# Kernel tuning notes

Hardware: AMD Instinct MI355X
Metric: run time of the kernel (lower is better)

## Reference

```python
import jax, jax.numpy as jnp
import numpy as np

B, N, F_IN, F_OUT = 8, 2048, 256, 256


def setup_inputs() -> dict:
    key = jax.random.key(0)
    k1, k2, k3, k4 = jax.random.split(key, 4)
    x = jax.random.normal(k1, (B, N, F_IN), dtype=jnp.float32)
    adj = jax.random.uniform(k2, (B, N, N), dtype=jnp.float32)
    W = jax.random.normal(k3, (F_IN, F_OUT), dtype=jnp.float32) * (1.0 / np.sqrt(F_IN))
    b = jax.random.normal(k4, (F_OUT,), dtype=jnp.float32)
    return {"x": x, "adj": adj, "W": W, "b": b}


def reference(x, adj, W, b):
    # GCN with dense adjacency: A_hat = A + I (fill_value=1.0, improved=False)
    n = adj.shape[-1]
    adj = adj + jnp.eye(n, dtype=adj.dtype)[None, :, :]
    deg = adj.sum(axis=-1)                       # [B, N]
    deg_inv_sqrt = deg ** -0.5
    deg_inv_sqrt = jnp.where(jnp.isinf(deg_inv_sqrt), 0.0, deg_inv_sqrt)
    # D^{-1/2} A D^{-1/2} via row/col broadcast (same math as diag bmm)
    adj_norm = deg_inv_sqrt[:, :, None] * adj * deg_inv_sqrt[:, None, :]
    h = jnp.einsum('bnf,fo->bno', x, W)          # linear, no bias
    out = jnp.einsum('bnm,bmo->bno', adj_norm, h)
    return out + b
```

## Files before the change

kernel.cpp:

```cpp
#include <hip/hip_runtime.h>
#include <hip/hip_bf16.h>

#define BB 8
#define NN 2048
#define FF 256
#define NT (NN / 64)

typedef __attribute__((ext_vector_type(8))) short short8;
typedef __attribute__((ext_vector_type(4))) short short4v;
typedef __attribute__((ext_vector_type(4))) float f32x4;
typedef __hip_bfloat16 bf16;

__device__ inline short f2bf(float x) {
  unsigned u = __builtin_bit_cast(unsigned, x);
  unsigned r = (u + 0x7fffu + ((u >> 16) & 1u)) >> 16;
  return (short)r;
}

__device__ inline void gl2lds16(const void* g, void* l) {
  __builtin_amdgcn_global_load_lds((const __attribute__((address_space(1))) void*)g,
                                   (__attribute__((address_space(3))) void*)l, 16, 0, 0);
}

__global__ __launch_bounds__(256)
void degconv_wt_kernel(const float* __restrict__ adj, const float* __restrict__ W,
                       float* __restrict__ dis, bf16* __restrict__ WT,
                       bf16* __restrict__ adjBF) {
  if (blockIdx.x >= BB * NN / 4) {
    int t2 = (blockIdx.x - BB * NN / 4) * 256 + threadIdx.x;
    int k = t2 >> 6, oc = (t2 & 63) * 4;
    float4 v = *reinterpret_cast<const float4*>(W + (size_t)k * FF + oc);
    *reinterpret_cast<short*>(WT + (size_t)(oc + 0) * FF + k) = f2bf(v.x);
    *reinterpret_cast<short*>(WT + (size_t)(oc + 1) * FF + k) = f2bf(v.y);
    *reinterpret_cast<short*>(WT + (size_t)(oc + 2) * FF + k) = f2bf(v.z);
    *reinterpret_cast<short*>(WT + (size_t)(oc + 3) * FF + k) = f2bf(v.w);
    return;
  }
  int wid = threadIdx.x >> 6, lane = threadIdx.x & 63;
  int row = blockIdx.x * 4 + wid;
  const float4* a4 = reinterpret_cast<const float4*>(adj + (size_t)row * NN);
  float4 v[8];
  float s = 0.f;
#pragma unroll
  for (int i = 0; i < 4; i++) {
    v[2 * i]     = a4[i * 128 + 2 * lane];
    v[2 * i + 1] = a4[i * 128 + 2 * lane + 1];
    s += v[2*i].x + v[2*i].y + v[2*i].z + v[2*i].w
       + v[2*i+1].x + v[2*i+1].y + v[2*i+1].z + v[2*i+1].w;
  }
#pragma unroll
  for (int off = 1; off < 64; off <<= 1) s += __shfl_xor(s, off, 64);
  float d = rsqrtf(s + 1.0f);
  if (lane == 0) dis[row] = d;
  int rb = row & (NN - 1);
#pragma unroll
  for (int i = 0; i < 8; i++) {
    int dd = rb - ((i >> 1) * 512 + 8 * lane + 4 * (i & 1));
    v[i].x += (dd == 0) ? 1.0f : 0.0f;
    v[i].y += (dd == 1) ? 1.0f : 0.0f;
    v[i].z += (dd == 2) ? 1.0f : 0.0f;
    v[i].w += (dd == 3) ? 1.0f : 0.0f;
  }
  bf16* orow = adjBF + (size_t)row * NN;
#pragma unroll
  for (int i = 0; i < 4; i++) {
    short8 w;
    w[0] = f2bf(v[2*i].x * d);   w[1] = f2bf(v[2*i].y * d);
    w[2] = f2bf(v[2*i].z * d);   w[3] = f2bf(v[2*i].w * d);
    w[4] = f2bf(v[2*i+1].x * d); w[5] = f2bf(v[2*i+1].y * d);
    w[6] = f2bf(v[2*i+1].z * d); w[7] = f2bf(v[2*i+1].w * d);
    *reinterpret_cast<short8*>(orow + i * 512 + 8 * lane) = w;
  }
}

__global__ __launch_bounds__(256)
void gemm1_kernel(const float* __restrict__ x, const bf16* __restrict__ WT,
                  const float* __restrict__ dis, bf16* __restrict__ gT) {
  __shared__ bf16 lA[128][40];
  __shared__ bf16 lB[128][40];
  int bid = blockIdx.x;
  int mtile = bid & 127, otile = bid >> 7;
  int m0 = mtile * 128, o0 = otile * 128;
  int t = threadIdx.x, wid = t >> 6, lane = t & 63;
  int wr = wid >> 1, wc = wid & 1;
  int srow = t >> 1, sseg = t & 1;
  const int r16 = lane & 15, kb = lane >> 4;

  f32x4 acc[4][4];
#pragma unroll
  for (int i = 0; i < 4; i++)
#pragma unroll
    for (int j = 0; j < 4; j++) acc[i][j] = (f32x4){0.f, 0.f, 0.f, 0.f};

  for (int k0 = 0; k0 < FF; k0 += 32) {
    {
      const float4* ap = reinterpret_cast<const float4*>(
          x + (size_t)(m0 + srow) * FF + k0 + sseg * 16);
      float arr[16];
      float4 v0 = ap[0], v1 = ap[1], v2 = ap[2], v3 = ap[3];
      arr[0]=v0.x; arr[1]=v0.y; arr[2]=v0.z; arr[3]=v0.w;
      arr[4]=v1.x; arr[5]=v1.y; arr[6]=v1.z; arr[7]=v1.w;
      arr[8]=v2.x; arr[9]=v2.y; arr[10]=v2.z; arr[11]=v2.w;
      arr[12]=v3.x; arr[13]=v3.y; arr[14]=v3.z; arr[15]=v3.w;
      short8 w0, w1;
#pragma unroll
      for (int e = 0; e < 8; e++) { w0[e] = f2bf(arr[e]); w1[e] = f2bf(arr[8 + e]); }
      *reinterpret_cast<short8*>(&lA[srow][sseg * 16]) = w0;
      *reinterpret_cast<short8*>(&lA[srow][sseg * 16 + 8]) = w1;
    }
    {
      const short8* bp = reinterpret_cast<const short8*>(
          WT + (size_t)(o0 + srow) * FF + k0 + sseg * 16);
      *reinterpret_cast<short8*>(&lB[srow][sseg * 16]) = bp[0];
      *reinterpret_cast<short8*>(&lB[srow][sseg * 16 + 8]) = bp[1];
    }
    __syncthreads();
    short8 af[4], bfr[4];
#pragma unroll
    for (int mf = 0; mf < 4; mf++)
      af[mf] = *reinterpret_cast<const short8*>(&lA[wr * 64 + mf * 16 + r16][kb * 8]);
#pragma unroll
    for (int nf = 0; nf < 4; nf++)
      bfr[nf] = *reinterpret_cast<const short8*>(&lB[wc * 64 + nf * 16 + r16][kb * 8]);
#pragma unroll
    for (int mf = 0; mf < 4; mf++)
#pragma unroll
      for (int nf = 0; nf < 4; nf++)
        acc[mf][nf] = __builtin_amdgcn_mfma_f32_16x16x32_bf16(af[mf], bfr[nf], acc[mf][nf], 0, 0, 0);
    __syncthreads();
  }

  int b = m0 >> 11;
#pragma unroll
  for (int mf = 0; mf < 4; mf++) {
    int mloc = wr * 64 + mf * 16 + (lane >> 4) * 4;
    int mg = m0 + mloc;
    float4 d4 = *reinterpret_cast<const float4*>(dis + mg);
#pragma unroll
    for (int nf = 0; nf < 4; nf++) {
      int o = o0 + wc * 64 + nf * 16 + r16;
      f32x4 v = acc[mf][nf];
      short4v w;
      w[0] = f2bf(v[0] * d4.x); w[1] = f2bf(v[1] * d4.y);
      w[2] = f2bf(v[2] * d4.z); w[3] = f2bf(v[3] * d4.w);
      *reinterpret_cast<short4v*>(gT + ((size_t)b * FF + o) * NN + (mg & (NN - 1))) = w;
    }
  }
}

__global__ __launch_bounds__(256, 4)
void gemm2_kernel(const bf16* __restrict__ adjBF, const bf16* __restrict__ gT,
                  const float* __restrict__ bias, float* __restrict__ out) {
  __shared__ __align__(16) bf16 lA[2][64 * 64];
  __shared__ __align__(16) bf16 lB[2][64 * 64];
  int bid = blockIdx.x;
  int x3 = bid & 7, idx = bid >> 3;
  int ob = idx & 3, hi = idx >> 2;
  int gg = hi * 8 + x3;
  int batch = gg >> 5, mtile = gg & 31;
  int n0 = mtile * 64, o0 = ob * 64;
  const bf16* Ab = adjBF + ((size_t)batch * NN + n0) * NN;
  const bf16* Bt = gT + ((size_t)batch * FF + o0) * NN;

  int t = threadIdx.x, wid = t >> 6, lane = t & 63;
  int wr = wid >> 1, wc = wid & 1;
  const int r16 = lane & 15, kb = lane >> 4;
  int trow = t >> 3, tslot = t & 7;

  f32x4 acc[2][2];
#pragma unroll
  for (int i = 0; i < 2; i++)
#pragma unroll
    for (int j = 0; j < 2; j++) acc[i][j] = (f32x4){0.f, 0.f, 0.f, 0.f};

  auto stage = [&](int buf, int ks) {
    bf16* la = &lA[buf][wid * 512];
    bf16* lb = &lB[buf][wid * 512];
#pragma unroll
    for (int q = 0; q < 2; q++) {
      int r = q * 32 + trow;
      int gs = tslot ^ (r & 7);
      gl2lds16(Ab + (size_t)r * NN + ks * 64 + 8 * gs, la + q * 2048);
      gl2lds16(Bt + (size_t)r * NN + ks * 64 + 8 * gs, lb + q * 2048);
    }
  };

  stage(0, 0);
  __syncthreads();
  int cur = 0;
#pragma unroll 1
  for (int ks = 0; ks < NT; ++ks) {
    if (ks + 1 < NT) stage(cur ^ 1, ks + 1);
    const bf16* sa = lA[cur];
    const bf16* sb = lB[cur];
    short8 af[2][2], bfr[2][2];
#pragma unroll
    for (int kk = 0; kk < 2; kk++) {
#pragma unroll
      for (int mf = 0; mf < 2; mf++) {
        int ra = wr * 32 + mf * 16 + r16;
        int slot = ((kk << 2) | kb) ^ (ra & 7);
        af[kk][mf] = *reinterpret_cast<const short8*>(&sa[ra * 64 + slot * 8]);
      }
#pragma unroll
      for (int nf = 0; nf < 2; nf++) {
        int rbr = wc * 32 + nf * 16 + r16;
        int slot = ((kk << 2) | kb) ^ (rbr & 7);
        bfr[kk][nf] = *reinterpret_cast<const short8*>(&sb[rbr * 64 + slot * 8]);
      }
    }
    __builtin_amdgcn_s_setprio(1);
#pragma unroll
    for (int kk = 0; kk < 2; kk++)
#pragma unroll
      for (int mf = 0; mf < 2; mf++)
#pragma unroll
        for (int nf = 0; nf < 2; nf++)
          acc[mf][nf] = __builtin_amdgcn_mfma_f32_16x16x32_bf16(
              af[kk][mf], bfr[kk][nf], acc[mf][nf], 0, 0, 0);
    __builtin_amdgcn_s_setprio(0);
    __syncthreads();
    cur ^= 1;
  }

  float bv[2];
#pragma unroll
  for (int nf = 0; nf < 2; nf++) bv[nf] = bias[o0 + wc * 32 + nf * 16 + r16];
#pragma unroll
  for (int mf = 0; mf < 2; mf++) {
    int ng = n0 + wr * 32 + mf * 16 + (lane >> 4) * 4;
    float* op0 = out + ((size_t)batch * NN + ng) * FF;
#pragma unroll
    for (int nf = 0; nf < 2; nf++) {
      int o = o0 + wc * 32 + nf * 16 + r16;
      f32x4 v = acc[mf][nf];
      op0[0 * FF + o] = v[0] + bv[nf];
      op0[1 * FF + o] = v[1] + bv[nf];
      op0[2 * FF + o] = v[2] + bv[nf];
      op0[3 * FF + o] = v[3] + bv[nf];
    }
  }
}

extern "C" void kernel_launch(void* const* d_in, const int* in_sizes, int n_in,
                              void* d_out, int out_size, void* d_ws, size_t ws_size,
                              hipStream_t stream) {
  const float* x    = (const float*)d_in[0];
  const float* adj  = (const float*)d_in[1];
  const float* W    = (const float*)d_in[2];
  const float* bias = (const float*)d_in[3];
  float* out = (float*)d_out;

  char* ws = (char*)d_ws;
  float* dis  = (float*)ws;
  bf16* WT    = (bf16*)(ws + (64 << 10));
  bf16* gT    = (bf16*)(ws + (192 << 10));
  bf16* adjBF = (bf16*)(ws + (192 << 10) + (8 << 20));

  degconv_wt_kernel<<<BB * NN / 4 + 64, 256, 0, stream>>>(adj, W, dis, WT, adjBF);
  gemm1_kernel<<<256, 256, 0, stream>>>(x, WT, dis, gT);
  gemm2_kernel<<<1024, 256, 0, stream>>>(adjBF, gT, bias, out);
}
```

Baseline: 76.33 us.

## Fuse adjacency bf16 conversion and identity add into aggregation GEMM

Drops the separate pass that wrote a normalized bf16 copy of the adjacency. The aggregation GEMM now reads the fp32 adjacency directly, adds the self-loop on the diagonal tile, converts to bf16 in registers and stores it to a swizzled LDS tile. The row degree scaling moves into the epilogue. This removes a 64MB write and re-read of the bf16 copy. In exchange the GEMM reads twice the bytes per A tile, once for each output-column block, and A staging now goes through registers rather than async global-to-LDS loads.

```diff
diff --git a/kernel.cpp b/kernel.cpp
--- a/kernel.cpp
+++ b/kernel.cpp
@@ -23,9 +23,8 @@
 }
 
 __global__ __launch_bounds__(256)
-void degconv_wt_kernel(const float* __restrict__ adj, const float* __restrict__ W,
-                       float* __restrict__ dis, bf16* __restrict__ WT,
-                       bf16* __restrict__ adjBF) {
+void deg_wt_kernel(const float* __restrict__ adj, const float* __restrict__ W,
+                   float* __restrict__ dis, bf16* __restrict__ WT) {
   if (blockIdx.x >= BB * NN / 4) {
     int t2 = (blockIdx.x - BB * NN / 4) * 256 + threadIdx.x;
     int k = t2 >> 6, oc = (t2 & 63) * 4;
@@ -40,37 +39,18 @@
   int row = blockIdx.x * 4 + wid;
   const float4* a4 = reinterpret_cast<const float4*>(adj + (size_t)row * NN);
   float4 v[8];
-  float s = 0.f;
 #pragma unroll
   for (int i = 0; i < 4; i++) {
     v[2 * i]     = a4[i * 128 + 2 * lane];
     v[2 * i + 1] = a4[i * 128 + 2 * lane + 1];
-    s += v[2*i].x + v[2*i].y + v[2*i].z + v[2*i].w
-       + v[2*i+1].x + v[2*i+1].y + v[2*i+1].z + v[2*i+1].w;
-  }
+  }
+  float s = 0.f;
+#pragma unroll
+  for (int i = 0; i < 8; i++)
+    s += v[i].x + v[i].y + v[i].z + v[i].w;
 #pragma unroll
   for (int off = 1; off < 64; off <<= 1) s += __shfl_xor(s, off, 64);
-  float d = rsqrtf(s + 1.0f);
-  if (lane == 0) dis[row] = d;
-  int rb = row & (NN - 1);
-#pragma unroll
-  for (int i = 0; i < 8; i++) {
-    int dd = rb - ((i >> 1) * 512 + 8 * lane + 4 * (i & 1));
-    v[i].x += (dd == 0) ? 1.0f : 0.0f;
-    v[i].y += (dd == 1) ? 1.0f : 0.0f;
-    v[i].z += (dd == 2) ? 1.0f : 0.0f;
-    v[i].w += (dd == 3) ? 1.0f : 0.0f;
-  }
-  bf16* orow = adjBF + (size_t)row * NN;
-#pragma unroll
-  for (int i = 0; i < 4; i++) {
-    short8 w;
-    w[0] = f2bf(v[2*i].x * d);   w[1] = f2bf(v[2*i].y * d);
-    w[2] = f2bf(v[2*i].z * d);   w[3] = f2bf(v[2*i].w * d);
-    w[4] = f2bf(v[2*i+1].x * d); w[5] = f2bf(v[2*i+1].y * d);
-    w[6] = f2bf(v[2*i+1].z * d); w[7] = f2bf(v[2*i+1].w * d);
-    *reinterpret_cast<short8*>(orow + i * 512 + 8 * lane) = w;
-  }
+  if (lane == 0) dis[row] = rsqrtf(s + 1.0f);
 }
 
 __global__ __launch_bounds__(256)
@@ -149,8 +129,9 @@
 }
 
 __global__ __launch_bounds__(256, 4)
-void gemm2_kernel(const bf16* __restrict__ adjBF, const bf16* __restrict__ gT,
-                  const float* __restrict__ bias, float* __restrict__ out) {
+void gemm2_kernel(const float* __restrict__ adj, const bf16* __restrict__ gT,
+                  const float* __restrict__ dis, const float* __restrict__ bias,
+                  float* __restrict__ out) {
   __shared__ __align__(16) bf16 lA[2][64 * 64];
   __shared__ __align__(16) bf16 lB[2][64 * 64];
   int bid = blockIdx.x;
@@ -159,13 +140,17 @@
   int gg = hi * 8 + x3;
   int batch = gg >> 5, mtile = gg & 31;
   int n0 = mtile * 64, o0 = ob * 64;
-  const bf16* Ab = adjBF + ((size_t)batch * NN + n0) * NN;
+  const float* Ab = adj + ((size_t)batch * NN + n0) * NN;
   const bf16* Bt = gT + ((size_t)batch * FF + o0) * NN;
+  const int dk = n0 >> 6;
 
   int t = threadIdx.x, wid = t >> 6, lane = t & 63;
   int wr = wid >> 1, wc = wid & 1;
   const int r16 = lane & 15, kb = lane >> 4;
   int trow = t >> 3, tslot = t & 7;
+  int arow = t >> 2, aq = t & 3;
+
+  const float4* arp = reinterpret_cast<const float4*>(Ab + (size_t)arow * NN);
 
   f32x4 acc[2][2];
 #pragma unroll
@@ -173,24 +158,52 @@
 #pragma unroll
     for (int j = 0; j < 2; j++) acc[i][j] = (f32x4){0.f, 0.f, 0.f, 0.f};
 
-  auto stage = [&](int buf, int ks) {
-    bf16* la = &lA[buf][wid * 512];
-    bf16* lb = &lB[buf][wid * 512];
+  float4 ar0, ar1, ar2, ar3;
+  auto loadA = [&](int ks) {
+    ar0 = arp[ks * 16 + aq * 4 + 0];
+    ar1 = arp[ks * 16 + aq * 4 + 1];
+    ar2 = arp[ks * 16 + aq * 4 + 2];
+    ar3 = arp[ks * 16 + aq * 4 + 3];
+  };
+  auto stageB = [&](int buf, int ks) {
 #pragma unroll
     for (int q = 0; q < 2; q++) {
       int r = q * 32 + trow;
       int gs = tslot ^ (r & 7);
-      gl2lds16(Ab + (size_t)r * NN + ks * 64 + 8 * gs, la + q * 2048);
-      gl2lds16(Bt + (size_t)r * NN + ks * 64 + 8 * gs, lb + q * 2048);
+      gl2lds16(Bt + (size_t)r * NN + ks * 64 + 8 * gs,
+               &lB[buf][q * 2048 + wid * 512]);
     }
   };
-
-  stage(0, 0);
+  auto convA = [&](int buf, int ks) {
+    if (ks == dk && (arow >> 4) == aq) {
+      int e = arow & 15;
+      ar0.x += (e == 0);  ar0.y += (e == 1);  ar0.z += (e == 2);  ar0.w += (e == 3);
+      ar1.x += (e == 4);  ar1.y += (e == 5);  ar1.z += (e == 6);  ar1.w += (e == 7);
+      ar2.x += (e == 8);  ar2.y += (e == 9);  ar2.z += (e == 10); ar2.w += (e == 11);
+      ar3.x += (e == 12); ar3.y += (e == 13); ar3.z += (e == 14); ar3.w += (e == 15);
+    }
+    short8 w0, w1;
+    w0[0] = f2bf(ar0.x); w0[1] = f2bf(ar0.y); w0[2] = f2bf(ar0.z); w0[3] = f2bf(ar0.w);
+    w0[4] = f2bf(ar1.x); w0[5] = f2bf(ar1.y); w0[6] = f2bf(ar1.z); w0[7] = f2bf(ar1.w);
+    w1[0] = f2bf(ar2.x); w1[1] = f2bf(ar2.y); w1[2] = f2bf(ar2.z); w1[3] = f2bf(ar2.w);
+    w1[4] = f2bf(ar3.x); w1[5] = f2bf(ar3.y); w1[6] = f2bf(ar3.z); w1[7] = f2bf(ar3.w);
+    int s0 = (aq * 2) ^ (arow & 7);
+    int s1 = (aq * 2 + 1) ^ (arow & 7);
+    *reinterpret_cast<short8*>(&lA[buf][arow * 64 + s0 * 8]) = w0;
+    *reinterpret_cast<short8*>(&lA[buf][arow * 64 + s1 * 8]) = w1;
+  };
+
+  loadA(0);
+  stageB(0, 0);
+  convA(0, 0);
   __syncthreads();
+
   int cur = 0;
 #pragma unroll 1
   for (int ks = 0; ks < NT; ++ks) {
-    if (ks + 1 < NT) stage(cur ^ 1, ks + 1);
+    bool more = (ks + 1 < NT);
+    int nxt = cur ^ 1;
+    if (more) { loadA(ks + 1); stageB(nxt, ks + 1); }
     const bf16* sa = lA[cur];
     const bf16* sb = lB[cur];
     short8 af[2][2], bfr[2][2];
@@ -219,25 +232,28 @@
           acc[mf][nf] = __builtin_amdgcn_mfma_f32_16x16x32_bf16(
               af[kk][mf], bfr[kk][nf], acc[mf][nf], 0, 0, 0);
     __builtin_amdgcn_s_setprio(0);
+    if (more) convA(nxt, ks + 1);
     __syncthreads();
-    cur ^= 1;
-  }
-
+    cur = nxt;
+  }
+
+  const float* disb = dis + (size_t)batch * NN;
   float bv[2];
 #pragma unroll
   for (int nf = 0; nf < 2; nf++) bv[nf] = bias[o0 + wc * 32 + nf * 16 + r16];
 #pragma unroll
   for (int mf = 0; mf < 2; mf++) {
     int ng = n0 + wr * 32 + mf * 16 + (lane >> 4) * 4;
+    float4 d4 = *reinterpret_cast<const float4*>(disb + ng);
     float* op0 = out + ((size_t)batch * NN + ng) * FF;
 #pragma unroll
     for (int nf = 0; nf < 2; nf++) {
       int o = o0 + wc * 32 + nf * 16 + r16;
       f32x4 v = acc[mf][nf];
-      op0[0 * FF + o] = v[0] + bv[nf];
-      op0[1 * FF + o] = v[1] + bv[nf];
-      op0[2 * FF + o] = v[2] + bv[nf];
-      op0[3 * FF + o] = v[3] + bv[nf];
+      op0[0 * FF + o] = v[0] * d4.x + bv[nf];
+      op0[1 * FF + o] = v[1] * d4.y + bv[nf];
+      op0[2 * FF + o] = v[2] * d4.z + bv[nf];
+      op0[3 * FF + o] = v[3] * d4.w + bv[nf];
     }
   }
 }
@@ -252,12 +268,11 @@
   float* out = (float*)d_out;
 
   char* ws = (char*)d_ws;
-  float* dis  = (float*)ws;
-  bf16* WT    = (bf16*)(ws + (64 << 10));
-  bf16* gT    = (bf16*)(ws + (192 << 10));
-  bf16* adjBF = (bf16*)(ws + (192 << 10) + (8 << 20));
-
-  degconv_wt_kernel<<<BB * NN / 4 + 64, 256, 0, stream>>>(adj, W, dis, WT, adjBF);
+  float* dis = (float*)ws;
+  bf16* WT   = (bf16*)(ws + (64 << 10));
+  bf16* gT   = (bf16*)(ws + (192 << 10));
+
+  deg_wt_kernel<<<BB * NN / 4 + 64, 256, 0, stream>>>(adj, W, dis, WT);
   gemm1_kernel<<<256, 256, 0, stream>>>(x, WT, dis, gT);
-  gemm2_kernel<<<1024, 256, 0, stream>>>(adjBF, gT, bias, out);
-}
+  gemm2_kernel<<<1024, 256, 0, stream>>>(adj, gT, dis, bias, out);
+}
```

Measured after the change: 98.98 us. 29.7% more time.

## Split degree pass from bf16 conversion and co-schedule conversion with gemm1

Applied to the files above, without the earlier changes.

The first kernel now only computes row degrees and the transposed bf16 weights. The normalized adjacency conversion moves into extra blocks of the gemm1 launch so it runs concurrently with the feature GEMM. This overlaps gemm1 with the conversion, but it requires reading the fp32 adjacency twice, roughly doubling that traffic unless the cache absorbs it.

```diff
diff --git a/kernel.cpp b/kernel.cpp
--- a/kernel.cpp
+++ b/kernel.cpp
@@ -23,9 +23,8 @@
 }
 
 __global__ __launch_bounds__(256)
-void degconv_wt_kernel(const float* __restrict__ adj, const float* __restrict__ W,
-                       float* __restrict__ dis, bf16* __restrict__ WT,
-                       bf16* __restrict__ adjBF) {
+void deg_wt_kernel(const float* __restrict__ adj, const float* __restrict__ W,
+                   float* __restrict__ dis, bf16* __restrict__ WT) {
   if (blockIdx.x >= BB * NN / 4) {
     int t2 = (blockIdx.x - BB * NN / 4) * 256 + threadIdx.x;
     int k = t2 >> 6, oc = (t2 & 63) * 4;
@@ -40,42 +39,56 @@
   int row = blockIdx.x * 4 + wid;
   const float4* a4 = reinterpret_cast<const float4*>(adj + (size_t)row * NN);
   float4 v[8];
-  float s = 0.f;
 #pragma unroll
   for (int i = 0; i < 4; i++) {
     v[2 * i]     = a4[i * 128 + 2 * lane];
     v[2 * i + 1] = a4[i * 128 + 2 * lane + 1];
-    s += v[2*i].x + v[2*i].y + v[2*i].z + v[2*i].w
-       + v[2*i+1].x + v[2*i+1].y + v[2*i+1].z + v[2*i+1].w;
-  }
+  }
+  float s = 0.f;
+#pragma unroll
+  for (int i = 0; i < 8; i++)
+    s += v[i].x + v[i].y + v[i].z + v[i].w;
 #pragma unroll
   for (int off = 1; off < 64; off <<= 1) s += __shfl_xor(s, off, 64);
-  float d = rsqrtf(s + 1.0f);
-  if (lane == 0) dis[row] = d;
-  int rb = row & (NN - 1);
-#pragma unroll
-  for (int i = 0; i < 8; i++) {
-    int dd = rb - ((i >> 1) * 512 + 8 * lane + 4 * (i & 1));
-    v[i].x += (dd == 0) ? 1.0f : 0.0f;
-    v[i].y += (dd == 1) ? 1.0f : 0.0f;
-    v[i].z += (dd == 2) ? 1.0f : 0.0f;
-    v[i].w += (dd == 3) ? 1.0f : 0.0f;
-  }
-  bf16* orow = adjBF + (size_t)row * NN;
-#pragma unroll
-  for (int i = 0; i < 4; i++) {
-    short8 w;
-    w[0] = f2bf(v[2*i].x * d);   w[1] = f2bf(v[2*i].y * d);
-    w[2] = f2bf(v[2*i].z * d);   w[3] = f2bf(v[2*i].w * d);
-    w[4] = f2bf(v[2*i+1].x * d); w[5] = f2bf(v[2*i+1].y * d);
-    w[6] = f2bf(v[2*i+1].z * d); w[7] = f2bf(v[2*i+1].w * d);
-    *reinterpret_cast<short8*>(orow + i * 512 + 8 * lane) = w;
-  }
+  if (lane == 0) dis[row] = rsqrtf(s + 1.0f);
 }
 
 __global__ __launch_bounds__(256)
-void gemm1_kernel(const float* __restrict__ x, const bf16* __restrict__ WT,
-                  const float* __restrict__ dis, bf16* __restrict__ gT) {
+void conv_gemm1_kernel(const float* __restrict__ adj, const float* __restrict__ x,
+                       const bf16* __restrict__ WT, const float* __restrict__ dis,
+                       bf16* __restrict__ gT, bf16* __restrict__ adjBF) {
+  if (blockIdx.x >= 256) {
+    int wid = threadIdx.x >> 6, lane = threadIdx.x & 63;
+    int row = (blockIdx.x - 256) * 4 + wid;
+    const float4* a4 = reinterpret_cast<const float4*>(adj + (size_t)row * NN);
+    float4 v[8];
+#pragma unroll
+    for (int i = 0; i < 4; i++) {
+      v[2 * i]     = a4[i * 128 + 2 * lane];
+      v[2 * i + 1] = a4[i * 128 + 2 * lane + 1];
+    }
+    float d = dis[row];
+    int rb = row & (NN - 1);
+#pragma unroll
+    for (int i = 0; i < 8; i++) {
+      int dd = rb - ((i >> 1) * 512 + 8 * lane + 4 * (i & 1));
+      v[i].x += (dd == 0) ? 1.0f : 0.0f;
+      v[i].y += (dd == 1) ? 1.0f : 0.0f;
+      v[i].z += (dd == 2) ? 1.0f : 0.0f;
+      v[i].w += (dd == 3) ? 1.0f : 0.0f;
+    }
+    bf16* orow = adjBF + (size_t)row * NN;
+#pragma unroll
+    for (int i = 0; i < 4; i++) {
+      short8 w;
+      w[0] = f2bf(v[2*i].x * d);   w[1] = f2bf(v[2*i].y * d);
+      w[2] = f2bf(v[2*i].z * d);   w[3] = f2bf(v[2*i].w * d);
+      w[4] = f2bf(v[2*i+1].x * d); w[5] = f2bf(v[2*i+1].y * d);
+      w[6] = f2bf(v[2*i+1].z * d); w[7] = f2bf(v[2*i+1].w * d);
+      *reinterpret_cast<short8*>(orow + i * 512 + 8 * lane) = w;
+    }
+    return;
+  }
   __shared__ bf16 lA[128][40];
   __shared__ bf16 lB[128][40];
   int bid = blockIdx.x;
@@ -257,7 +270,7 @@
   bf16* gT    = (bf16*)(ws + (192 << 10));
   bf16* adjBF = (bf16*)(ws + (192 << 10) + (8 << 20));
 
-  degconv_wt_kernel<<<BB * NN / 4 + 64, 256, 0, stream>>>(adj, W, dis, WT, adjBF);
-  gemm1_kernel<<<256, 256, 0, stream>>>(x, WT, dis, gT);
+  deg_wt_kernel<<<BB * NN / 4 + 64, 256, 0, stream>>>(adj, W, dis, WT);
+  conv_gemm1_kernel<<<256 + BB * NN / 4, 256, 0, stream>>>(adj, x, WT, dis, gT, adjBF);
   gemm2_kernel<<<1024, 256, 0, stream>>>(adjBF, gT, bias, out);
 }
```

Result: slower. 88.51 us (+15.9%).
